# Optimization experiments

Hardware: AMD Instinct MI355X
Metric: run time of the kernel (lower is better)

The kernel has to match this reference:

```python
import jax, jax.numpy as jnp
import numpy as np

B, T = 4, 512
V, D, L, H, F = 32000, 1024, 12, 16, 4096
HD = D // H
CUTS = [0, 2000, 8000, V]
SHRINK = 4


def layer_norm(x, s, b, eps=1e-5):
    m = jnp.mean(x, axis=-1, keepdims=True)
    v = jnp.var(x, axis=-1, keepdims=True)
    return (x - m) * jax.lax.rsqrt(v + eps) * s + b


def rel_shift(x):
    # Transformer-XL relative shift. x: [B, H, T, S] with S == T.
    b, h, t, s = x.shape
    x = jnp.pad(x, ((0, 0), (0, 0), (0, 0), (1, 0)))
    x = x.reshape(b, h, s + 1, t)[:, :, 1:, :]
    return x.reshape(b, h, t, s)


def sinusoid_pos_emb(seq_len, dim):
    # positions seq_len-1 ... 0 (TXL convention), [seq_len, dim]
    pos = jnp.arange(seq_len - 1, -1, -1.0, dtype=jnp.float32)
    inv_freq = 1.0 / (10000.0 ** (jnp.arange(0, dim, 2, dtype=jnp.float32) / dim))
    ang = pos[:, None] * inv_freq[None, :]
    return jnp.concatenate([jnp.sin(ang), jnp.cos(ang)], axis=-1)


def setup_inputs() -> dict:
    key = jax.random.key(0)
    ks = iter(jax.random.split(key, 64))

    def n(shape, std=0.02):
        return jax.random.normal(next(ks), shape, dtype=jnp.float32) * std

    hids = [D // (SHRINK ** i) for i in range(3)]  # 1024, 256, 64
    inp = {}
    inp['x'] = jax.random.randint(next(ks), (B, T), 0, V)
    inp['emb_0'] = n([CUTS[1] - CUTS[0], hids[0]])
    inp['emb_1'] = n([CUTS[2] - CUTS[1], hids[1]])
    inp['emb_2'] = n([CUTS[3] - CUTS[2], hids[2]])
    inp['proj_1'] = n([hids[1], D], 0.01)
    inp['proj_2'] = n([hids[2], D], 0.01)
    inp['out_bias'] = jnp.zeros([V], jnp.float32)
    inp['r_w_bias'] = n([1, 1, H, HD])
    inp['r_r_bias'] = n([1, 1, H, HD])
    inp['ln1_s'] = jnp.ones([L, D], jnp.float32)
    inp['ln1_b'] = jnp.zeros([L, D], jnp.float32)
    inp['Wq'] = n([L, D, D]); inp['bq'] = jnp.zeros([L, D], jnp.float32)
    inp['Wk'] = n([L, D, D]); inp['bk'] = jnp.zeros([L, D], jnp.float32)
    inp['Wv'] = n([L, D, D]); inp['bv'] = jnp.zeros([L, D], jnp.float32)
    inp['Wr'] = n([L, D, D])  # relative position projection (no bias)
    inp['Wo'] = n([L, D, D]); inp['bo'] = jnp.zeros([L, D], jnp.float32)
    inp['ln2_s'] = jnp.ones([L, D], jnp.float32)
    inp['ln2_b'] = jnp.zeros([L, D], jnp.float32)
    inp['W1'] = n([L, D, F]); inp['b1'] = jnp.zeros([L, F], jnp.float32)
    inp['W2'] = n([L, F, D]); inp['b2'] = jnp.zeros([L, D], jnp.float32)
    return inp


def forward(x, emb_0, emb_1, emb_2, proj_1, proj_2, out_bias, r_w_bias, r_r_bias,
            ln1_s, ln1_b, Wq, bq, Wk, bk, Wv, bv, Wr, Wo, bo, ln2_s, ln2_b,
            W1, b1, W2, b2):
    Bx, Tx = x.shape
    # --- adaptive input embedding (clustered table + up-projection, scaled) ---
    embs = [emb_0, emb_1, emb_2]
    projs = [None, proj_1, proj_2]
    h = jnp.zeros((Bx, Tx, D), jnp.float32)
    for i in range(3):
        lo, hi = CUTS[i], CUTS[i + 1]
        in_bucket = (x >= lo) & (x < hi)
        idx = jnp.clip(x - lo, 0, hi - lo - 1)
        e = embs[i][idx]  # [B, T, hid_i]
        if projs[i] is not None:
            e = e @ projs[i]  # -> [B, T, D]
        h = h + jnp.where(in_bucket[..., None], e, 0.0)
    h = h * jnp.sqrt(jnp.float32(D))

    pemb = sinusoid_pos_emb(Tx, D)                  # [T, D]
    causal = jnp.tril(jnp.ones((Tx, Tx), bool))     # [T, T]
    scale = 1.0 / np.sqrt(HD)

    for i in range(L):
        # --- TXL relative-position multi-head attention (pre-norm) ---
        a_in = layer_norm(h, ln1_s[i], ln1_b[i])
        q = (a_in @ Wq[i] + bq[i]).reshape(Bx, Tx, H, HD)
        k = (a_in @ Wk[i] + bk[i]).reshape(Bx, Tx, H, HD)
        v = (a_in @ Wv[i] + bv[i]).reshape(Bx, Tx, H, HD)
        r_k = (pemb @ Wr[i]).reshape(Tx, H, HD)     # [T, H, HD]
        content = jnp.einsum('bthd,bshd->bhts', q + r_w_bias[0, 0], k)
        rel = jnp.einsum('bthd,shd->bhts', q + r_r_bias[0, 0], r_k)
        logits = (content + rel_shift(rel)) * scale
        logits = jnp.where(causal[None, None], logits, jnp.float32(-1e30))
        attn = jax.nn.softmax(logits, axis=-1)
        o = jnp.einsum('bhts,bshd->bthd', attn, v).reshape(Bx, Tx, D)
        h = h + (o @ Wo[i] + bo[i])
        # --- FFN (pre-norm, GELU) ---
        f_in = layer_norm(h, ln2_s[i], ln2_b[i])
        h = h + (jax.nn.gelu(f_in @ W1[i] + b1[i]) @ W2[i] + b2[i])

    # --- tied adaptive-softmax output projection ---
    W_full = jnp.concatenate([emb_0, emb_1 @ proj_1, emb_2 @ proj_2], axis=0)  # [V, D]
    return h @ W_full.T + out_bias  # [B, T, V]


def reference(x, emb_0, emb_1, emb_2, proj_1, proj_2, out_bias, r_w_bias, r_r_bias,
              ln1_s, ln1_b, Wq, bq, Wk, bk, Wv, bv, Wr, Wo, bo, ln2_s, ln2_b,
              W1, b1, W2, b2):
    return forward(x, emb_0, emb_1, emb_2, proj_1, proj_2, out_bias, r_w_bias,
                   r_r_bias, ln1_s, ln1_b, Wq, bq, Wk, bk, Wv, bv, Wr, Wo, bo,
                   ln2_s, ln2_b, W1, b1, W2, b2)
```

## Files before the change

### kernel.cpp

```cpp
#include <hip/hip_runtime.h>

using us = unsigned short;
typedef short short8v __attribute__((ext_vector_type(8)));
typedef float float4v __attribute__((ext_vector_type(4)));

constexpr int NB  = 4;
constexpr int NT  = 512;
constexpr int ND  = 1024;
constexpr int NL  = 12;
constexpr int NH  = 16;
constexpr int NF  = 4096;
constexpr int NHD = 64;
constexpr int NBT = NB * NT;
constexpr int NV  = 32000;
constexpr long QOFF = (long)NBT * ND;
constexpr long RKL  = 640L * 1024;

__device__ __forceinline__ us f2bf(float f) {
    unsigned u = __float_as_uint(f);
    u += 0x7fffu + ((u >> 16) & 1u);
    return (us)(u >> 16);
}

__device__ __forceinline__ void gload16(const us* g, us* l) {
    __builtin_amdgcn_global_load_lds(
        (const __attribute__((address_space(1))) void*)g,
        (__attribute__((address_space(3))) void*)l, 16, 0, 0);
}

template<int BM, int BN, int EPI, bool OUTBF>
__global__ __launch_bounds__(256)
void bgemm_k(const us* __restrict__ A, const us* __restrict__ B, void* Cv,
             const float* __restrict__ bias, const float* addsrc,
             const float* __restrict__ p0, const float* __restrict__ p1,
             us* __restrict__ vtp,
             int N, int K, int lda, int ldb, int ldc,
             int bdiv, long sAb, long sAh, long sBb, long sBh, long sCb, long sCh)
{
    constexpr int BK  = 64;
    constexpr int WTM = BM / 2, WTN = BN / 2;
    constexpr int FM  = WTM / 16, FN = WTN / 16;
    constexpr int AI  = BM / 32;
    constexpr int BI  = BN / 32;
    static_assert(BM % 32 == 0 && BN % 32 == 0, "");

    long coff = 0;
    if (bdiv > 0) {
        int z = blockIdx.z, zb = z / bdiv, zh = z % bdiv;
        A += zb * sAb + zh * sAh;
        B += zb * sBb + zh * sBh;
        coff = zb * sCb + zh * sCh;
    }
    float* Cf = (float*)Cv + coff;
    us*    Ch = (us*)Cv + coff;
    if (addsrc) addsrc += coff;

    __shared__ __align__(16) us As[2 * BM * BK];
    __shared__ __align__(16) us Bs[2 * BN * BK];

    const int tid  = threadIdx.x;
    const int lane = tid & 63;
    const int w    = tid >> 6;
    const int wm   = w >> 1;
    const int wn   = w & 1;
    const int row0 = blockIdx.y * BM;
    const int col0 = blockIdx.x * BN;

    float4v acc[FM][FN];
#pragma unroll
    for (int i = 0; i < FM; ++i)
#pragma unroll
        for (int j = 0; j < FN; ++j) acc[i][j] = (float4v)0.f;

    auto stage = [&](int buf, int k0) {
        us* Ad = As + buf * (BM * BK);
        us* Bd = Bs + buf * (BN * BK);
#pragma unroll
        for (int i = 0; i < AI; ++i) {
            int rb = w * (BM / 4) + i * 8;
            int r  = rb + (lane >> 3);
            int sc8 = ((lane & 7) ^ (r & 7)) << 3;
            gload16(A + (long)(row0 + r) * lda + k0 + sc8, Ad + rb * 64);
        }
#pragma unroll
        for (int i = 0; i < BI; ++i) {
            int rb = w * (BN / 4) + i * 8;
            int r  = rb + (lane >> 3);
            int sc8 = ((lane & 7) ^ (r & 7)) << 3;
            gload16(B + (long)(col0 + r) * ldb + k0 + sc8, Bd + rb * 64);
        }
    };

    stage(0, 0);
    __syncthreads();
    int cur = 0;
    for (int k0 = 0; k0 < K; k0 += BK) {
        if (k0 + BK < K) stage(cur ^ 1, k0 + BK);
        const char* Ac = (const char*)(As + cur * (BM * BK));
        const char* Bc = (const char*)(Bs + cur * (BN * BK));
#pragma unroll
        for (int ks = 0; ks < 2; ++ks) {
            short8v af[FM], bfr[FN];
            int sw = ks * 4 + (lane >> 4);
#pragma unroll
            for (int i = 0; i < FM; ++i) {
                int r = wm * WTM + i * 16 + (lane & 15);
                af[i] = *reinterpret_cast<const short8v*>(Ac + r * 128 + ((sw ^ (r & 7)) << 4));
            }
#pragma unroll
            for (int j = 0; j < FN; ++j) {
                int r = wn * WTN + j * 16 + (lane & 15);
                bfr[j] = *reinterpret_cast<const short8v*>(Bc + r * 128 + ((sw ^ (r & 7)) << 4));
            }
#pragma unroll
            for (int i = 0; i < FM; ++i)
#pragma unroll
                for (int j = 0; j < FN; ++j)
                    acc[i][j] = __builtin_amdgcn_mfma_f32_16x16x32_bf16(af[i], bfr[j], acc[i][j], 0, 0, 0);
        }
        __syncthreads();
        cur ^= 1;
    }

#pragma unroll
    for (int i = 0; i < FM; ++i) {
        int growb = row0 + wm * WTM + i * 16 + ((lane >> 4) << 2);
#pragma unroll
        for (int j = 0; j < FN; ++j) {
            int gcol = col0 + wn * WTN + j * 16 + (lane & 15);
            if (EPI == 3) {
                int seg = gcol >> 10, c = gcol & 1023;
                float bb = bias[gcol];
                if (seg == 2) {
                    unsigned lo = (unsigned)f2bf(acc[i][j][0] + bb)
                                | ((unsigned)f2bf(acc[i][j][1] + bb) << 16);
                    unsigned hi = (unsigned)f2bf(acc[i][j][2] + bb)
                                | ((unsigned)f2bf(acc[i][j][3] + bb) << 16);
                    int bidx = growb >> 9, tb = growb & 511;
                    uint2 pk; pk.x = lo; pk.y = hi;
                    *reinterpret_cast<uint2*>(
                        vtp + ((long)((bidx * 16 + (c >> 6)) * 64 + (c & 63)) << 9) + tb) = pk;
                } else {
                    us* base = (us*)Cv;
#pragma unroll
                    for (int r = 0; r < 4; ++r) {
                        int gr = growb + r;
                        float v = acc[i][j][r] + bb;
                        long o = (long)gr * 1024 + c;
                        if (seg == 0) {
                            base[o]        = f2bf(v + p0[c]);
                            base[o + QOFF] = f2bf(v + p1[c]);
                        } else base[o + 2 * QOFF] = f2bf(v);
                    }
                }
            } else {
                if (gcol >= N) continue;
#pragma unroll
                for (int r = 0; r < 4; ++r) {
                    int gr = growb + r;
                    float v = acc[i][j][r];
                    if (bias) v += bias[gcol];
                    if (EPI == 1) {
                        float xx = v;
                        v = 0.5f * xx * (1.f + tanhf(0.7978845608028654f
                                                     * (xx + 0.044715f * xx * xx * xx)));
                    }
                    if (addsrc) v += addsrc[(long)gr * ldc + gcol];
                    if (OUTBF) Ch[(long)gr * ldc + gcol] = f2bf(v);
                    else       Cf[(long)gr * ldc + gcol] = v;
                }
            }
        }
    }
}

template<int NPART, int MODE>
__global__ __launch_bounds__(256)
void redln_k(const float* __restrict__ part, const float* __restrict__ bias,
             float* __restrict__ h, us* __restrict__ outb,
             const float* __restrict__ sc, const float* __restrict__ bi)
{
    int row = blockIdx.x;
    int d4 = threadIdx.x * 4;
    long i = (long)row * ND + d4;
    float4 hv = *reinterpret_cast<const float4*>(h + i);
    float4 bb = *reinterpret_cast<const float4*>(bias + d4);
    hv.x += bb.x; hv.y += bb.y; hv.z += bb.z; hv.w += bb.w;
#pragma unroll
    for (int z = 0; z < NPART; ++z) {
        float4 a = *reinterpret_cast<const float4*>(part + (long)z * 2097152 + i);
        hv.x += a.x; hv.y += a.y; hv.z += a.z; hv.w += a.w;
    }
    *reinterpret_cast<float4*>(h + i) = hv;
    if (MODE == 1) {
        uint2 p;
        p.x = (unsigned)f2bf(hv.x) | ((unsigned)f2bf(hv.y) << 16);
        p.y = (unsigned)f2bf(hv.z) | ((unsigned)f2bf(hv.w) << 16);
        *reinterpret_cast<uint2*>(outb + i) = p;
    } else {
        float sum = hv.x + hv.y + hv.z + hv.w;
        float sq  = hv.x * hv.x + hv.y * hv.y + hv.z * hv.z + hv.w * hv.w;
#pragma unroll
        for (int o = 32; o; o >>= 1) { sum += __shfl_xor(sum, o); sq += __shfl_xor(sq, o); }
        __shared__ float red[8];
        int w = threadIdx.x >> 6;
        if ((threadIdx.x & 63) == 0) { red[w] = sum; red[4 + w] = sq; }
        __syncthreads();
        sum = red[0] + red[1] + red[2] + red[3];
        sq  = red[4] + red[5] + red[6] + red[7];
        float mean = sum * (1.f / ND);
        float var  = fmaxf(sq * (1.f / ND) - mean * mean, 0.f);
        float inv  = rsqrtf(var + 1e-5f);
        float4 s4 = *reinterpret_cast<const float4*>(&sc[d4]);
        float4 b4 = *reinterpret_cast<const float4*>(&bi[d4]);
        uint2 p;
        p.x = (unsigned)f2bf((hv.x - mean) * inv * s4.x + b4.x)
            | ((unsigned)f2bf((hv.y - mean) * inv * s4.y + b4.y) << 16);
        p.y = (unsigned)f2bf((hv.z - mean) * inv * s4.z + b4.z)
            | ((unsigned)f2bf((hv.w - mean) * inv * s4.w + b4.w) << 16);
        *reinterpret_cast<uint2*>(outb + i) = p;
    }
}

__global__ __launch_bounds__(256)
void fattn_k(const us* __restrict__ qkv, const us* __restrict__ vt,
             const us* __restrict__ rk, us* __restrict__ obuf)
{
    __shared__ __align__(16) us lds_k[64 * 64];
    __shared__ __align__(16) us lds_v[64 * 64];
    __shared__ __align__(16) us lds_rk[64 * 64];
    __shared__ __align__(16) us lds_p[4 * 16 * 64];
    __shared__ float lds_r[4 * 16 * 132];

    const int tid = threadIdx.x, lane = tid & 63, w = tid >> 6;
    const int qtp = blockIdx.x, bh = blockIdx.y;
    const int b = bh >> 4, h = bh & 15;
    const int rg = lane >> 4, lc = lane & 15;

    const us* qwb = qkv + ((long)b * 512) * 1024 + h * 64;
    const us* qrb = qwb + QOFF;
    const us* kb  = qwb + 2 * QOFF;
    const us* vtb = vt + (long)bh * 64 * 512;
    const us* rkb = rk + h * 64;

    float* rbase = lds_r + w * (16 * 132);
    us*    pbase = lds_p + w * (16 * 64);

    for (int hh = 0; hh < 2; ++hh) {
        const int qt = hh ? 7 - qtp : qtp;
        const int t0 = qt * 64;

        short8v aqw[2], aqr[2];
        {
            long qrow = (long)(t0 + w * 16 + lc) * 1024;
            int ko = rg * 8;
            aqw[0] = *(const short8v*)(qwb + qrow + ko);
            aqw[1] = *(const short8v*)(qwb + qrow + 32 + ko);
            aqr[0] = *(const short8v*)(qrb + qrow + ko);
            aqr[1] = *(const short8v*)(qrb + qrow + 32 + ko);
        }

        float4v oacc[4];
#pragma unroll
        for (int i = 0; i < 4; ++i) oacc[i] = (float4v)0.f;
        float mrow[4] = {-3e38f, -3e38f, -3e38f, -3e38f};
        float lrow[4] = {0.f, 0.f, 0.f, 0.f};

        auto stage_rk = [&](int j0) {
#pragma unroll
            for (int i = 0; i < 2; ++i) {
                int rb = w * 16 + i * 8;
                int r  = rb + (lane >> 3);
                int sl = ((lane & 7) ^ (r & 7)) << 3;
                gload16(rkb + (long)(j0 + r) * 1024 + sl, lds_rk + rb * 64);
            }
        };
        auto rel_half = [&](int wbase) {
#pragma unroll
            for (int jn = 0; jn < 4; ++jn) {
                float4v rf = (float4v)0.f;
#pragma unroll
                for (int kk = 0; kk < 2; ++kk) {
                    int r = jn * 16 + lc;
                    int sw = kk * 4 + rg;
                    short8v bf = *(const short8v*)((const char*)lds_rk + r * 128 + ((sw ^ (r & 7)) << 4));
                    rf = __builtin_amdgcn_mfma_f32_16x16x32_bf16(aqr[kk], bf, rf, 0, 0, 0);
                }
#pragma unroll
                for (int pr = 0; pr < 4; ++pr)
                    rbase[(rg * 4 + pr) * 132 + wbase + jn * 16 + lc] = rf[pr];
            }
        };

        const int nst = qt + 1;
        for (int st = 0; st < nst; ++st) {
            const int s0 = st * 64;
            const int jb = (st - qt) * 64 + 448;
            const int sb = ((st - qt + 7) & 1) << 6;

#pragma unroll
            for (int i = 0; i < 2; ++i) {
                int rb = w * 16 + i * 8;
                int r  = rb + (lane >> 3);
                int sl = ((lane & 7) ^ (r & 7)) << 3;
                gload16(kb + (long)(s0 + r) * 1024 + sl, lds_k + rb * 64);
                gload16(vtb + (long)r * 512 + s0 + sl, lds_v + rb * 64);
            }
            if (st == 0) {
                stage_rk(jb);
                __syncthreads();
                rel_half(sb);
                __syncthreads();
                stage_rk(jb + 64);
                __syncthreads();
            } else {
                stage_rk(jb + 64);
                __syncthreads();
            }

            float4v sfr[4];
#pragma unroll
            for (int sn = 0; sn < 4; ++sn) {
                sfr[sn] = (float4v)0.f;
#pragma unroll
                for (int kk = 0; kk < 2; ++kk) {
                    int r = sn * 16 + lc;
                    int sw = kk * 4 + rg;
                    short8v bf = *(const short8v*)((const char*)lds_k + r * 128 + ((sw ^ (r & 7)) << 4));
                    sfr[sn] = __builtin_amdgcn_mfma_f32_16x16x32_bf16(aqw[kk], bf, sfr[sn], 0, 0, 0);
                }
            }
            rel_half(sb ^ 64);

            float pv[4][4];
            float rmax[4] = {-3e38f, -3e38f, -3e38f, -3e38f};
#pragma unroll
            for (int pr = 0; pr < 4; ++pr) {
                int tt = rg * 4 + pr;
                int tw = w * 16 + tt;
#pragma unroll
                for (int sn = 0; sn < 4; ++sn) {
                    int ss = sn * 16 + lc;
                    int slot = (sb + ss + 63 - tw) & 127;
                    float lg = (sfr[sn][pr] + rbase[tt * 132 + slot]) * 0.125f;
                    if (ss > t0 - s0 + tw) lg = -1e30f;
                    pv[sn][pr] = lg;
                    rmax[pr] = fmaxf(rmax[pr], lg);
                }
            }
#pragma unroll
            for (int o = 1; o < 16; o <<= 1)
#pragma unroll
                for (int pr = 0; pr < 4; ++pr)
                    rmax[pr] = fmaxf(rmax[pr], __shfl_xor(rmax[pr], o));
            float rsum[4];
#pragma unroll
            for (int pr = 0; pr < 4; ++pr) {
                float mn = fmaxf(mrow[pr], rmax[pr]);
                float al = __expf(mrow[pr] - mn);
                mrow[pr] = mn;
                lrow[pr] *= al;
                float s = 0.f;
#pragma unroll
                for (int sn = 0; sn < 4; ++sn) {
                    float p = __expf(pv[sn][pr] - mn);
                    pv[sn][pr] = p;
                    s += p;
                }
                rsum[pr] = s;
#pragma unroll
                for (int dn = 0; dn < 4; ++dn) oacc[dn][pr] *= al;
            }
#pragma unroll
            for (int o = 1; o < 16; o <<= 1)
#pragma unroll
                for (int pr = 0; pr < 4; ++pr)
                    rsum[pr] += __shfl_xor(rsum[pr], o);
#pragma unroll
            for (int pr = 0; pr < 4; ++pr) lrow[pr] += rsum[pr];

#pragma unroll
            for (int pr = 0; pr < 4; ++pr) {
                int row = rg * 4 + pr;
#pragma unroll
                for (int sn = 0; sn < 4; ++sn) {
                    int col = sn * 16 + lc;
                    *(us*)((char*)pbase + row * 128 + (((col >> 3) ^ (row & 7)) << 4) + (col & 7) * 2)
                        = f2bf(pv[sn][pr]);
                }
            }
            short8v pa[2];
#pragma unroll
            for (int kk = 0; kk < 2; ++kk)
                pa[kk] = *(const short8v*)((const char*)pbase + lc * 128 + (((kk * 4 + rg) ^ (lc & 7)) << 4));
#pragma unroll
            for (int dn = 0; dn < 4; ++dn) {
#pragma unroll
                for (int kk = 0; kk < 2; ++kk) {
                    int r = dn * 16 + lc;
                    int sw = kk * 4 + rg;
                    short8v vb = *(const short8v*)((const char*)lds_v + r * 128 + ((sw ^ (r & 7)) << 4));
                    oacc[dn] = __builtin_amdgcn_mfma_f32_16x16x32_bf16(pa[kk], vb, oacc[dn], 0, 0, 0);
                }
            }
            __syncthreads();
        }
#pragma unroll
        for (int pr = 0; pr < 4; ++pr) {
            int t = t0 + w * 16 + rg * 4 + pr;
            float inv = 1.f / lrow[pr];
            long rowo = ((long)b * 512 + t) * 1024 + h * 64;
#pragma unroll
            for (int dn = 0; dn < 4; ++dn)
                obuf[rowo + dn * 16 + lc] = f2bf(oacc[dn][pr] * inv);
        }
    }
}

__global__ __launch_bounds__(256)
void tconv_k(const float* __restrict__ in, us* __restrict__ out, int R, int C,
             long inL, long outL)
{
    in  += (long)blockIdx.z * inL;
    out += (long)blockIdx.z * outL;
    __shared__ float t[32][33];
    int c0 = blockIdx.x * 32, r0 = blockIdx.y * 32;
    int tx = threadIdx.x & 31, ty = threadIdx.x >> 5;
#pragma unroll
    for (int j = 0; j < 4; ++j)
        t[ty + j * 8][tx] = in[(long)(r0 + ty + j * 8) * C + c0 + tx];
    __syncthreads();
#pragma unroll
    for (int j = 0; j < 4; ++j)
        out[(long)(c0 + ty + j * 8) * R + r0 + tx] = f2bf(t[tx][ty + j * 8]);
}

__global__ __launch_bounds__(256)
void conv_k(const float* __restrict__ in, us* __restrict__ out, long n)
{
    long i = ((long)blockIdx.x * 256 + threadIdx.x) * 4;
    if (i >= n) return;
    float4 v = *reinterpret_cast<const float4*>(in + i);
    uint2 p;
    p.x = (unsigned)f2bf(v.x) | ((unsigned)f2bf(v.y) << 16);
    p.y = (unsigned)f2bf(v.z) | ((unsigned)f2bf(v.w) << 16);
    *reinterpret_cast<uint2*>(out + i) = p;
}

__global__ __launch_bounds__(256)
void rkpad12_k(us* __restrict__ rk)
{
    int i = blockIdx.x * 256 + threadIdx.x;
    int l = i >> 13, r = i & 8191;
    reinterpret_cast<uint4*>(rk + (long)l * RKL + 512 * 1024)[r] = make_uint4(0, 0, 0, 0);
}

__global__ __launch_bounds__(256)
void bcat_k(const float* __restrict__ bq, const float* __restrict__ bk,
            const float* __restrict__ bv, float* __restrict__ o)
{
    int i = blockIdx.x * 256 + threadIdx.x;
    int l = i / 3072, rr = i % 3072, seg = rr >> 10, c = rr & 1023;
    const float* s = seg == 0 ? bq : seg == 1 ? bk : bv;
    o[i] = s[l * 1024 + c];
}

__global__ __launch_bounds__(256)
void ln_k(const float* __restrict__ x, us* __restrict__ y,
          const float* __restrict__ sc, const float* __restrict__ bi)
{
    int row = blockIdx.x;
    const float* xr = x + (long)row * ND;
    int d4 = threadIdx.x * 4;
    float4 v = *reinterpret_cast<const float4*>(&xr[d4]);
    float sum = v.x + v.y + v.z + v.w;
    float sq  = v.x * v.x + v.y * v.y + v.z * v.z + v.w * v.w;
#pragma unroll
    for (int o = 32; o; o >>= 1) { sum += __shfl_xor(sum, o); sq += __shfl_xor(sq, o); }
    __shared__ float red[8];
    int w = threadIdx.x >> 6;
    if ((threadIdx.x & 63) == 0) { red[w] = sum; red[4 + w] = sq; }
    __syncthreads();
    sum = red[0] + red[1] + red[2] + red[3];
    sq  = red[4] + red[5] + red[6] + red[7];
    float mean = sum * (1.f / ND);
    float var  = fmaxf(sq * (1.f / ND) - mean * mean, 0.f);
    float inv  = rsqrtf(var + 1e-5f);
    float4 s4 = *reinterpret_cast<const float4*>(&sc[d4]);
    float4 b4 = *reinterpret_cast<const float4*>(&bi[d4]);
    uint2 p;
    p.x = (unsigned)f2bf((v.x - mean) * inv * s4.x + b4.x)
        | ((unsigned)f2bf((v.y - mean) * inv * s4.y + b4.y) << 16);
    p.y = (unsigned)f2bf((v.z - mean) * inv * s4.z + b4.z)
        | ((unsigned)f2bf((v.w - mean) * inv * s4.w + b4.w) << 16);
    *reinterpret_cast<uint2*>(y + (long)row * ND + d4) = p;
}

__global__ __launch_bounds__(256)
void pemb_k(us* __restrict__ p)
{
    int t = blockIdx.x;
    float pos = (float)(NT - 1 - t);
    for (int j = threadIdx.x; j < ND / 2; j += 256) {
        float invf = expf(-(float)j * (9.210340371976184f / 512.0f));
        float ang  = pos * invf;
        p[(long)t * ND + j]           = f2bf(sinf(ang));
        p[(long)t * ND + ND / 2 + j]  = f2bf(cosf(ang));
    }
}

__global__ __launch_bounds__(256)
void embed_k(const int* __restrict__ x,
             const float* __restrict__ e0, const float* __restrict__ e1,
             const float* __restrict__ e2, const float* __restrict__ p1,
             const float* __restrict__ p2, float* __restrict__ h)
{
    __shared__ float e[256];
    int tok = blockIdx.x;
    int v = x[tok];
    float* outp = h + (long)tok * ND;
    if (v < 2000) {
        const float* r = e0 + (long)v * ND;
        for (int d = threadIdx.x; d < ND; d += 256) outp[d] = r[d] * 32.0f;
    } else if (v < 8000) {
        const float* r = e1 + (long)(v - 2000) * 256;
        e[threadIdx.x] = r[threadIdx.x];
        __syncthreads();
        for (int d = threadIdx.x; d < ND; d += 256) {
            float acc = 0.f;
#pragma unroll 4
            for (int i = 0; i < 256; ++i) acc += e[i] * p1[(long)i * ND + d];
            outp[d] = acc * 32.0f;
        }
    } else {
        const float* r = e2 + (long)(v - 8000) * 64;
        if (threadIdx.x < 64) e[threadIdx.x] = r[threadIdx.x];
        __syncthreads();
        for (int d = threadIdx.x; d < ND; d += 256) {
            float acc = 0.f;
#pragma unroll 4
            for (int i = 0; i < 64; ++i) acc += e[i] * p2[(long)i * ND + d];
            outp[d] = acc * 32.0f;
        }
    }
}

extern "C" void kernel_launch(void* const* d_in, const int* in_sizes, int n_in,
                              void* d_out, int out_size, void* d_ws, size_t ws_size,
                              hipStream_t stream)
{
    (void)in_sizes; (void)n_in; (void)out_size;
    const int*   x     = (const int*)  d_in[0];
    const float* emb0  = (const float*)d_in[1];
    const float* emb1  = (const float*)d_in[2];
    const float* emb2  = (const float*)d_in[3];
    const float* proj1 = (const float*)d_in[4];
    const float* proj2 = (const float*)d_in[5];
    const float* obias = (const float*)d_in[6];
    const float* rwb   = (const float*)d_in[7];
    const float* rrb   = (const float*)d_in[8];
    const float* ln1s  = (const float*)d_in[9];
    const float* ln1b  = (const float*)d_in[10];
    const float* Wq    = (const float*)d_in[11];
    const float* bq    = (const float*)d_in[12];
    const float* Wk    = (const float*)d_in[13];
    const float* bk    = (const float*)d_in[14];
    const float* Wv    = (const float*)d_in[15];
    const float* bv    = (const float*)d_in[16];
    const float* Wr    = (const float*)d_in[17];
    const float* Wo    = (const float*)d_in[18];
    const float* bo    = (const float*)d_in[19];
    const float* ln2s  = (const float*)d_in[20];
    const float* ln2b  = (const float*)d_in[21];
    const float* W1    = (const float*)d_in[22];
    const float* b1    = (const float*)d_in[23];
    const float* W2    = (const float*)d_in[24];
    const float* b2    = (const float*)d_in[25];
    float* out = (float*)d_out;

    us* ob      = (us*)out;
    us* qkvbuf  = ob;
    us* mid_bf  = ob +  6291456;
    us* vt_bf   = ob + 14680064;
    us* o_bf    = ob + 16777216;
    us* ain_bf  = ob + 18874368;
    us* rk_all  = ob + 20971520;
    us* pemb_bf = ob + 28835840;
    us* wqkv_sc = ob + 29360128;
    us* wr_sc   = ob + 32505856;
    us* wo_sc   = ob + 33554432;
    us* w1_sc   = ob + 34603008;
    us* w2_sc   = ob + 38797312;
    float* pffn = out + 21495808;
    float* pwo  = out + 29884416;

    float* wsf      = (float*)d_ws;
    float* h        = wsf;
    us*    h_bf     = (us*)(wsf + 2097152);
    us*    hp1_bf   = h_bf   + 2097152;
    us*    hp2_bf   = hp1_bf + 524288;
    us*    emb0_bf  = hp2_bf + 131072;
    us*    emb1_bf  = emb0_bf + 2097152;
    us*    emb2_bf  = emb1_bf + 1572864;
    us*    proj1_bf = emb2_bf + 1540096;
    us*    proj2_bf = proj1_bf + 262144;
    float* bqkv     = (float*)(proj2_bf + 65536);
    us*    wqkv_all = (us*)(bqkv + 36864);
    us*    wr_all   = wqkv_all + (long)NL * 3072 * 1024;
    us*    wo_all   = wr_all   + (long)NL * 1024 * 1024;
    us*    w1_all   = wo_all   + (long)NL * 1024 * 1024;
    us*    w2_all   = w1_all   + (long)NL * 4096 * 1024;
    const bool big  = ws_size >= (size_t)352273408;

    bcat_k<<<144, 256, 0, stream>>>(bq, bk, bv, bqkv);
    conv_k<<<2000, 256, 0, stream>>>(emb0,  emb0_bf,  2048000);
    conv_k<<<1500, 256, 0, stream>>>(emb1,  emb1_bf,  1536000);
    conv_k<<<1500, 256, 0, stream>>>(emb2,  emb2_bf,  1536000);
    conv_k<<<256,  256, 0, stream>>>(proj1, proj1_bf, 262144);
    conv_k<<<64,   256, 0, stream>>>(proj2, proj2_bf, 65536);
    pemb_k<<<NT, 256, 0, stream>>>(pemb_bf);
    rkpad12_k<<<384, 256, 0, stream>>>(rk_all);
    embed_k<<<NBT, 256, 0, stream>>>(x, emb0, emb1, emb2, proj1, proj2, h);
    if (big) {
        tconv_k<<<dim3(32, 32, NL), 256, 0, stream>>>(Wq, wqkv_all,           1024, 1024, 1048576, 3145728);
        tconv_k<<<dim3(32, 32, NL), 256, 0, stream>>>(Wk, wqkv_all + 1048576, 1024, 1024, 1048576, 3145728);
        tconv_k<<<dim3(32, 32, NL), 256, 0, stream>>>(Wv, wqkv_all + 2097152, 1024, 1024, 1048576, 3145728);
        tconv_k<<<dim3(32, 32, NL), 256, 0, stream>>>(Wr, wr_all, 1024, 1024, 1048576, 1048576);
        tconv_k<<<dim3(32, 32, NL), 256, 0, stream>>>(Wo, wo_all, 1024, 1024, 1048576, 1048576);
        tconv_k<<<dim3(128, 32, NL), 256, 0, stream>>>(W1, w1_all, 1024, 4096, 4194304, 4194304);
        tconv_k<<<dim3(32, 128, NL), 256, 0, stream>>>(W2, w2_all, 4096, 1024, 4194304, 4194304);
        bgemm_k<64, 64, 0, true><<<dim3(16, 8, NL), 256, 0, stream>>>(
            pemb_bf, wr_all, rk_all, nullptr, nullptr, nullptr, nullptr, nullptr,
            1024, 1024, 1024, 1024, 1024,
            1, 0, 0, 1048576, 0, RKL, 0);
    }
    ln_k<<<NBT, 256, 0, stream>>>(h, ain_bf, ln1s, ln1b);

    for (int l = 0; l < NL; ++l) {
        const us* wqkv_t = big ? wqkv_all + (long)l * 3145728 : wqkv_sc;
        const us* wo_t   = big ? wo_all   + (long)l * 1048576 : wo_sc;
        const us* w1_t   = big ? w1_all   + (long)l * 4194304 : w1_sc;
        const us* w2_t   = big ? w2_all   + (long)l * 4194304 : w2_sc;
        if (!big) {
            const long wOff = (long)l * ND * ND;
            tconv_k<<<dim3(32, 32), 256, 0, stream>>>(Wq + wOff, wqkv_sc,           1024, 1024, 0, 0);
            tconv_k<<<dim3(32, 32), 256, 0, stream>>>(Wk + wOff, wqkv_sc + 1048576, 1024, 1024, 0, 0);
            tconv_k<<<dim3(32, 32), 256, 0, stream>>>(Wv + wOff, wqkv_sc + 2097152, 1024, 1024, 0, 0);
            tconv_k<<<dim3(32, 32), 256, 0, stream>>>(Wr + wOff, wr_sc, 1024, 1024, 0, 0);
            tconv_k<<<dim3(32, 32), 256, 0, stream>>>(Wo + wOff, wo_sc, 1024, 1024, 0, 0);
            tconv_k<<<dim3(128, 32), 256, 0, stream>>>(W1 + (long)l * ND * NF, w1_sc, 1024, 4096, 0, 0);
            tconv_k<<<dim3(32, 128), 256, 0, stream>>>(W2 + (long)l * ND * NF, w2_sc, 4096, 1024, 0, 0);
            bgemm_k<64, 64, 0, true><<<dim3(16, 8, 1), 256, 0, stream>>>(
                pemb_bf, wr_sc, rk_all + (long)l * RKL, nullptr, nullptr, nullptr, nullptr, nullptr,
                1024, 1024, 1024, 1024, 1024, 0, 0, 0, 0, 0, 0, 0);
        }

        bgemm_k<128, 64, 3, true><<<dim3(48, 16, 1), 256, 0, stream>>>(
            ain_bf, wqkv_t, qkvbuf, bqkv + l * 3072, nullptr, rwb, rrb, vt_bf,
            3072, 1024, 1024, 1024, 1024, 0, 0, 0, 0, 0, 0, 0);
        fattn_k<<<dim3(4, NB * NH), 256, 0, stream>>>(
            qkvbuf, vt_bf, rk_all + (long)l * RKL, o_bf);
        bgemm_k<128, 64, 0, false><<<dim3(16, 16, 2), 256, 0, stream>>>(
            o_bf, wo_t, pwo, nullptr, nullptr, nullptr, nullptr, nullptr,
            1024, 512, 1024, 1024, 1024,
            1, 512, 0, 512, 0, 2097152, 0);
        redln_k<2, 0><<<NBT, 256, 0, stream>>>(
            pwo, bo + l * ND, h, ain_bf, ln2s + l * ND, ln2b + l * ND);

        bgemm_k<128, 128, 1, true><<<dim3(32, 16, 1), 256, 0, stream>>>(
            ain_bf, w1_t, mid_bf, b1 + (long)l * NF, nullptr, nullptr, nullptr, nullptr,
            4096, 1024, 1024, 1024, 4096, 0, 0, 0, 0, 0, 0, 0);
        bgemm_k<128, 128, 0, false><<<dim3(8, 16, 4), 256, 0, stream>>>(
            mid_bf, w2_t, pffn, nullptr, nullptr, nullptr, nullptr, nullptr,
            1024, 1024, 4096, 4096, 1024,
            1, 1024, 0, 1024, 0, 2097152, 0);
        if (l < NL - 1)
            redln_k<4, 0><<<NBT, 256, 0, stream>>>(
                pffn, b2 + (long)l * ND, h, ain_bf,
                ln1s + (l + 1) * ND, ln1b + (l + 1) * ND);
        else
            redln_k<4, 1><<<NBT, 256, 0, stream>>>(
                pffn, b2 + (long)l * ND, h, h_bf, nullptr, nullptr);
    }

    bgemm_k<128, 64, 0, false><<<dim3(32, 16, 1), 256, 0, stream>>>(
        h_bf, emb0_bf, out, obias, nullptr, nullptr, nullptr, nullptr,
        2000, 1024, 1024, 1024, NV, 0, 0, 0, 0, 0, 0, 0);
    bgemm_k<64, 64, 0, true><<<dim3(4, 32, 1), 256, 0, stream>>>(
        h_bf, proj1_bf, hp1_bf, nullptr, nullptr, nullptr, nullptr, nullptr,
        256, 1024, 1024, 1024, 256, 0, 0, 0, 0, 0, 0, 0);
    bgemm_k<128, 128, 0, false><<<dim3(47, 16, 1), 256, 0, stream>>>(
        hp1_bf, emb1_bf, out + 2000, obias + 2000, nullptr, nullptr, nullptr, nullptr,
        6000, 256, 256, 256, NV, 0, 0, 0, 0, 0, 0, 0);
    bgemm_k<64, 64, 0, true><<<dim3(1, 32, 1), 256, 0, stream>>>(
        h_bf, proj2_bf, hp2_bf, nullptr, nullptr, nullptr, nullptr, nullptr,
        64, 1024, 1024, 1024, 64, 0, 0, 0, 0, 0, 0, 0);
    bgemm_k<128, 128, 0, false><<<dim3(188, 16, 1), 256, 0, stream>>>(
        hp2_bf, emb2_bf, out + 8000, obias + 8000, nullptr, nullptr, nullptr, nullptr,
        24000, 64, 64, 64, NV, 0, 0, 0, 0, 0, 0, 0);
}
```

Baseline: 2.459 ms.

## Double-buffer K/V and triple-buffer RK tiles in flash attention, merge conversion kernels

The attention kernel now prefetches the next K/V tile and the next relative-key tile into alternate LDS buffers while the current tile is computed, so global loads overlap with MFMA work. This removes the per-iteration barriers that previously serialized load and compute. The five fp32-to-bf16 conversion launches are also merged into one kernel to cut launch overhead. LDS usage roughly doubles for K/V/RK, which may lower occupancy, and the loop relies on the trailing barrier for buffer reuse safety.

```diff
diff --git a/kernel.cpp b/kernel.cpp
--- a/kernel.cpp
+++ b/kernel.cpp
@@ -226,9 +226,9 @@
 void fattn_k(const us* __restrict__ qkv, const us* __restrict__ vt,
              const us* __restrict__ rk, us* __restrict__ obuf)
 {
-    __shared__ __align__(16) us lds_k[64 * 64];
-    __shared__ __align__(16) us lds_v[64 * 64];
-    __shared__ __align__(16) us lds_rk[64 * 64];
+    __shared__ __align__(16) us lds_k[2][64 * 64];
+    __shared__ __align__(16) us lds_v[2][64 * 64];
+    __shared__ __align__(16) us lds_rk[3][64 * 64];
     __shared__ __align__(16) us lds_p[4 * 16 * 64];
     __shared__ float lds_r[4 * 16 * 132];
 
@@ -245,6 +245,26 @@
 
     float* rbase = lds_r + w * (16 * 132);
     us*    pbase = lds_p + w * (16 * 64);
+
+    auto stage_kv = [&](int buf, int s0) {
+#pragma unroll
+        for (int i = 0; i < 2; ++i) {
+            int rb = w * 16 + i * 8;
+            int r  = rb + (lane >> 3);
+            int sl = ((lane & 7) ^ (r & 7)) << 3;
+            gload16(kb + (long)(s0 + r) * 1024 + sl, lds_k[buf] + rb * 64);
+            gload16(vtb + (long)r * 512 + s0 + sl, lds_v[buf] + rb * 64);
+        }
+    };
+    auto stage_rk = [&](int buf, int j0) {
+#pragma unroll
+        for (int i = 0; i < 2; ++i) {
+            int rb = w * 16 + i * 8;
+            int r  = rb + (lane >> 3);
+            int sl = ((lane & 7) ^ (r & 7)) << 3;
+            gload16(rkb + (long)(j0 + r) * 1024 + sl, lds_rk[buf] + rb * 64);
+        }
+    };
 
     for (int hh = 0; hh < 2; ++hh) {
         const int qt = hh ? 7 - qtp : qtp;
@@ -266,16 +286,7 @@
         float mrow[4] = {-3e38f, -3e38f, -3e38f, -3e38f};
         float lrow[4] = {0.f, 0.f, 0.f, 0.f};
 
-        auto stage_rk = [&](int j0) {
-#pragma unroll
-            for (int i = 0; i < 2; ++i) {
-                int rb = w * 16 + i * 8;
-                int r  = rb + (lane >> 3);
-                int sl = ((lane & 7) ^ (r & 7)) << 3;
-                gload16(rkb + (long)(j0 + r) * 1024 + sl, lds_rk + rb * 64);
-            }
-        };
-        auto rel_half = [&](int wbase) {
+        auto rel_half = [&](int buf, int wbase) {
 #pragma unroll
             for (int jn = 0; jn < 4; ++jn) {
                 float4v rf = (float4v)0.f;
@@ -283,7 +294,7 @@
                 for (int kk = 0; kk < 2; ++kk) {
                     int r = jn * 16 + lc;
                     int sw = kk * 4 + rg;
-                    short8v bf = *(const short8v*)((const char*)lds_rk + r * 128 + ((sw ^ (r & 7)) << 4));
+                    short8v bf = *(const short8v*)((const char*)lds_rk[buf] + r * 128 + ((sw ^ (r & 7)) << 4));
                     rf = __builtin_amdgcn_mfma_f32_16x16x32_bf16(aqr[kk], bf, rf, 0, 0, 0);
                 }
 #pragma unroll
@@ -292,32 +303,23 @@
             }
         };
 
-        const int nst = qt + 1;
-        for (int st = 0; st < nst; ++st) {
+        const int jb0 = 448 - qt * 64;
+        stage_kv(0, 0);
+        stage_rk(0, jb0);
+        stage_rk(1, jb0 + 64);
+        __syncthreads();
+
+        for (int st = 0; st <= qt; ++st) {
             const int s0 = st * 64;
-            const int jb = (st - qt) * 64 + 448;
             const int sb = ((st - qt + 7) & 1) << 6;
-
-#pragma unroll
-            for (int i = 0; i < 2; ++i) {
-                int rb = w * 16 + i * 8;
-                int r  = rb + (lane >> 3);
-                int sl = ((lane & 7) ^ (r & 7)) << 3;
-                gload16(kb + (long)(s0 + r) * 1024 + sl, lds_k + rb * 64);
-                gload16(vtb + (long)r * 512 + s0 + sl, lds_v + rb * 64);
-            }
-            if (st == 0) {
-                stage_rk(jb);
-                __syncthreads();
-                rel_half(sb);
-                __syncthreads();
-                stage_rk(jb + 64);
-                __syncthreads();
-            } else {
-                stage_rk(jb + 64);
-                __syncthreads();
-            }
-
+            if (st < qt) {
+                stage_kv((st + 1) & 1, s0 + 64);
+                stage_rk((st + 2) % 3, (st + 1 - qt) * 64 + 448 + 64);
+            }
+            if (st == 0) { rel_half(0, sb); rel_half(1, sb ^ 64); }
+            else         rel_half((st + 1) % 3, sb ^ 64);
+            const char* Kc = (const char*)lds_k[st & 1];
+            const char* Vc = (const char*)lds_v[st & 1];
             float4v sfr[4];
 #pragma unroll
             for (int sn = 0; sn < 4; ++sn) {
@@ -326,11 +328,10 @@
                 for (int kk = 0; kk < 2; ++kk) {
                     int r = sn * 16 + lc;
                     int sw = kk * 4 + rg;
-                    short8v bf = *(const short8v*)((const char*)lds_k + r * 128 + ((sw ^ (r & 7)) << 4));
+                    short8v bf = *(const short8v*)(Kc + r * 128 + ((sw ^ (r & 7)) << 4));
                     sfr[sn] = __builtin_amdgcn_mfma_f32_16x16x32_bf16(aqw[kk], bf, sfr[sn], 0, 0, 0);
                 }
             }
-            rel_half(sb ^ 64);
 
             float pv[4][4];
             float rmax[4] = {-3e38f, -3e38f, -3e38f, -3e38f};
@@ -399,7 +400,7 @@
                 for (int kk = 0; kk < 2; ++kk) {
                     int r = dn * 16 + lc;
                     int sw = kk * 4 + rg;
-                    short8v vb = *(const short8v*)((const char*)lds_v + r * 128 + ((sw ^ (r & 7)) << 4));
+                    short8v vb = *(const short8v*)(Vc + r * 128 + ((sw ^ (r & 7)) << 4));
                     oacc[dn] = __builtin_amdgcn_mfma_f32_16x16x32_bf16(pa[kk], vb, oacc[dn], 0, 0, 0);
                 }
             }
@@ -436,15 +437,25 @@
 }
 
 __global__ __launch_bounds__(256)
-void conv_k(const float* __restrict__ in, us* __restrict__ out, long n)
-{
-    long i = ((long)blockIdx.x * 256 + threadIdx.x) * 4;
-    if (i >= n) return;
-    float4 v = *reinterpret_cast<const float4*>(in + i);
+void convall_k(const float* __restrict__ e0, const float* __restrict__ e1,
+               const float* __restrict__ e2, const float* __restrict__ p1,
+               const float* __restrict__ p2,
+               us* __restrict__ d0, us* __restrict__ d1, us* __restrict__ d2,
+               us* __restrict__ d3, us* __restrict__ d4)
+{
+    int blk = blockIdx.x;
+    const float* s; us* d; long off;
+    if (blk < 2000)      { s = e0; d = d0; off = (long)blk * 1024; }
+    else if (blk < 3500) { s = e1; d = d1; off = (long)(blk - 2000) * 1024; }
+    else if (blk < 5000) { s = e2; d = d2; off = (long)(blk - 3500) * 1024; }
+    else if (blk < 5256) { s = p1; d = d3; off = (long)(blk - 5000) * 1024; }
+    else                 { s = p2; d = d4; off = (long)(blk - 5256) * 1024; }
+    long i = off + (long)threadIdx.x * 4;
+    float4 v = *reinterpret_cast<const float4*>(s + i);
     uint2 p;
     p.x = (unsigned)f2bf(v.x) | ((unsigned)f2bf(v.y) << 16);
     p.y = (unsigned)f2bf(v.z) | ((unsigned)f2bf(v.w) << 16);
-    *reinterpret_cast<uint2*>(out + i) = p;
+    *reinterpret_cast<uint2*>(d + i) = p;
 }
 
 __global__ __launch_bounds__(256)
@@ -613,11 +624,8 @@
     const bool big  = ws_size >= (size_t)352273408;
 
     bcat_k<<<144, 256, 0, stream>>>(bq, bk, bv, bqkv);
-    conv_k<<<2000, 256, 0, stream>>>(emb0,  emb0_bf,  2048000);
-    conv_k<<<1500, 256, 0, stream>>>(emb1,  emb1_bf,  1536000);
-    conv_k<<<1500, 256, 0, stream>>>(emb2,  emb2_bf,  1536000);
-    conv_k<<<256,  256, 0, stream>>>(proj1, proj1_bf, 262144);
-    conv_k<<<64,   256, 0, stream>>>(proj2, proj2_bf, 65536);
+    convall_k<<<5320, 256, 0, stream>>>(emb0, emb1, emb2, proj1, proj2,
+                                        emb0_bf, emb1_bf, emb2_bf, proj1_bf, proj2_bf);
     pemb_k<<<NT, 256, 0, stream>>>(pemb_bf);
     rkpad12_k<<<384, 256, 0, stream>>>(rk_all);
     embed_k<<<NBT, 256, 0, stream>>>(x, emb0, emb1, emb2, proj1, proj2, h);
```

Result: no change. 2.449 ms (-0.4%).

## Split attention KV range across two blocks and merge partial softmax results

Applied to the files above, without the earlier changes.

The flash attention kernel now splits each query tile's key range into two halves across a new grid dimension. Each block writes unnormalised fp32 partial outputs plus row max and sum, and a new merge kernel combines them into bf16 output. This doubles the attention grid from 256 blocks to fuller occupancy on the many-CU GPU, at the cost of extra fp32 global traffic and another launch per layer. Separately, the five embedding conversion launches are fused into a single kernel.

```diff
diff --git a/kernel.cpp b/kernel.cpp
--- a/kernel.cpp
+++ b/kernel.cpp
@@ -224,7 +224,8 @@
 
 __global__ __launch_bounds__(256)
 void fattn_k(const us* __restrict__ qkv, const us* __restrict__ vt,
-             const us* __restrict__ rk, us* __restrict__ obuf)
+             const us* __restrict__ rk, float* __restrict__ pO,
+             float* __restrict__ pm, float* __restrict__ pl)
 {
     __shared__ __align__(16) us lds_k[64 * 64];
     __shared__ __align__(16) us lds_v[64 * 64];
@@ -233,7 +234,7 @@
     __shared__ float lds_r[4 * 16 * 132];
 
     const int tid = threadIdx.x, lane = tid & 63, w = tid >> 6;
-    const int qtp = blockIdx.x, bh = blockIdx.y;
+    const int qtp = blockIdx.x, bh = blockIdx.y, hf = blockIdx.z;
     const int b = bh >> 4, h = bh & 15;
     const int rg = lane >> 4, lc = lane & 15;
 
@@ -246,9 +247,23 @@
     float* rbase = lds_r + w * (16 * 132);
     us*    pbase = lds_p + w * (16 * 64);
 
+    auto stage_rk = [&](int j0) {
+#pragma unroll
+        for (int i = 0; i < 2; ++i) {
+            int rb = w * 16 + i * 8;
+            int r  = rb + (lane >> 3);
+            int sl = ((lane & 7) ^ (r & 7)) << 3;
+            gload16(rkb + (long)(j0 + r) * 1024 + sl, lds_rk + rb * 64);
+        }
+    };
+
     for (int hh = 0; hh < 2; ++hh) {
         const int qt = hh ? 7 - qtp : qtp;
         const int t0 = qt * 64;
+        const int n  = qt + 1;
+        const int h0 = (n + 1) >> 1;
+        const int st_s = hf ? h0 : 0;
+        const int st_e = hf ? n  : h0;
 
         short8v aqw[2], aqr[2];
         {
@@ -266,15 +281,6 @@
         float mrow[4] = {-3e38f, -3e38f, -3e38f, -3e38f};
         float lrow[4] = {0.f, 0.f, 0.f, 0.f};
 
-        auto stage_rk = [&](int j0) {
-#pragma unroll
-            for (int i = 0; i < 2; ++i) {
-                int rb = w * 16 + i * 8;
-                int r  = rb + (lane >> 3);
-                int sl = ((lane & 7) ^ (r & 7)) << 3;
-                gload16(rkb + (long)(j0 + r) * 1024 + sl, lds_rk + rb * 64);
-            }
-        };
         auto rel_half = [&](int wbase) {
 #pragma unroll
             for (int jn = 0; jn < 4; ++jn) {
@@ -292,8 +298,7 @@
             }
         };
 
-        const int nst = qt + 1;
-        for (int st = 0; st < nst; ++st) {
+        for (int st = st_s; st < st_e; ++st) {
             const int s0 = st * 64;
             const int jb = (st - qt) * 64 + 448;
             const int sb = ((st - qt + 7) & 1) << 6;
@@ -306,7 +311,7 @@
                 gload16(kb + (long)(s0 + r) * 1024 + sl, lds_k + rb * 64);
                 gload16(vtb + (long)r * 512 + s0 + sl, lds_v + rb * 64);
             }
-            if (st == 0) {
+            if (st == st_s) {
                 stage_rk(jb);
                 __syncthreads();
                 rel_half(sb);
@@ -405,16 +410,36 @@
             }
             __syncthreads();
         }
+
 #pragma unroll
         for (int pr = 0; pr < 4; ++pr) {
             int t = t0 + w * 16 + rg * 4 + pr;
-            float inv = 1.f / lrow[pr];
-            long rowo = ((long)b * 512 + t) * 1024 + h * 64;
+            long rowi = (long)(hf * 64 + bh) * 512 + t;
+            float* od = pO + rowi * 64;
 #pragma unroll
             for (int dn = 0; dn < 4; ++dn)
-                obuf[rowo + dn * 16 + lc] = f2bf(oacc[dn][pr] * inv);
-        }
-    }
+                od[dn * 16 + lc] = oacc[dn][pr];
+            if (lc == 0) { pm[rowi] = mrow[pr]; pl[rowi] = lrow[pr]; }
+        }
+    }
+}
+
+__global__ __launch_bounds__(256)
+void amerge_k(const float* __restrict__ pO, const float* __restrict__ pm,
+              const float* __restrict__ pl, us* __restrict__ obuf)
+{
+    int row = blockIdx.x * 4 + (threadIdx.x >> 6);
+    int d   = threadIdx.x & 63;
+    float m0 = pm[row], m1 = pm[row + 32768];
+    float l0 = pl[row], l1 = pl[row + 32768];
+    float M  = fmaxf(m0, m1);
+    float a0 = __expf(m0 - M), a1 = __expf(m1 - M);
+    float L  = a0 * l0 + a1 * l1;
+    long i0 = (long)row * 64 + d;
+    float o = (a0 * pO[i0] + a1 * pO[i0 + 2097152]) / L;
+    int bh = row >> 9, t = row & 511;
+    int b = bh >> 4, h = bh & 15;
+    obuf[((long)(b * 512 + t)) * 1024 + h * 64 + d] = f2bf(o);
 }
 
 __global__ __launch_bounds__(256)
@@ -436,15 +461,25 @@
 }
 
 __global__ __launch_bounds__(256)
-void conv_k(const float* __restrict__ in, us* __restrict__ out, long n)
-{
-    long i = ((long)blockIdx.x * 256 + threadIdx.x) * 4;
-    if (i >= n) return;
-    float4 v = *reinterpret_cast<const float4*>(in + i);
+void convall_k(const float* __restrict__ e0, const float* __restrict__ e1,
+               const float* __restrict__ e2, const float* __restrict__ p1,
+               const float* __restrict__ p2,
+               us* __restrict__ d0, us* __restrict__ d1, us* __restrict__ d2,
+               us* __restrict__ d3, us* __restrict__ d4)
+{
+    int blk = blockIdx.x;
+    const float* s; us* d; long off;
+    if (blk < 2000)      { s = e0; d = d0; off = (long)blk * 1024; }
+    else if (blk < 3500) { s = e1; d = d1; off = (long)(blk - 2000) * 1024; }
+    else if (blk < 5000) { s = e2; d = d2; off = (long)(blk - 3500) * 1024; }
+    else if (blk < 5256) { s = p1; d = d3; off = (long)(blk - 5000) * 1024; }
+    else                 { s = p2; d = d4; off = (long)(blk - 5256) * 1024; }
+    long i = off + (long)threadIdx.x * 4;
+    float4 v = *reinterpret_cast<const float4*>(s + i);
     uint2 p;
     p.x = (unsigned)f2bf(v.x) | ((unsigned)f2bf(v.y) << 16);
     p.y = (unsigned)f2bf(v.z) | ((unsigned)f2bf(v.w) << 16);
-    *reinterpret_cast<uint2*>(out + i) = p;
+    *reinterpret_cast<uint2*>(d + i) = p;
 }
 
 __global__ __launch_bounds__(256)
@@ -593,6 +628,9 @@
     us* w2_sc   = ob + 38797312;
     float* pffn = out + 21495808;
     float* pwo  = out + 29884416;
+    float* pO   = out + 34078720;
+    float* pm   = out + 42467328;
+    float* pl   = out + 42532864;
 
     float* wsf      = (float*)d_ws;
     float* h        = wsf;
@@ -613,11 +651,8 @@
     const bool big  = ws_size >= (size_t)352273408;
 
     bcat_k<<<144, 256, 0, stream>>>(bq, bk, bv, bqkv);
-    conv_k<<<2000, 256, 0, stream>>>(emb0,  emb0_bf,  2048000);
-    conv_k<<<1500, 256, 0, stream>>>(emb1,  emb1_bf,  1536000);
-    conv_k<<<1500, 256, 0, stream>>>(emb2,  emb2_bf,  1536000);
-    conv_k<<<256,  256, 0, stream>>>(proj1, proj1_bf, 262144);
-    conv_k<<<64,   256, 0, stream>>>(proj2, proj2_bf, 65536);
+    convall_k<<<5320, 256, 0, stream>>>(emb0, emb1, emb2, proj1, proj2,
+                                        emb0_bf, emb1_bf, emb2_bf, proj1_bf, proj2_bf);
     pemb_k<<<NT, 256, 0, stream>>>(pemb_bf);
     rkpad12_k<<<384, 256, 0, stream>>>(rk_all);
     embed_k<<<NBT, 256, 0, stream>>>(x, emb0, emb1, emb2, proj1, proj2, h);
@@ -658,8 +693,9 @@
         bgemm_k<128, 64, 3, true><<<dim3(48, 16, 1), 256, 0, stream>>>(
             ain_bf, wqkv_t, qkvbuf, bqkv + l * 3072, nullptr, rwb, rrb, vt_bf,
             3072, 1024, 1024, 1024, 1024, 0, 0, 0, 0, 0, 0, 0);
-        fattn_k<<<dim3(4, NB * NH), 256, 0, stream>>>(
-            qkvbuf, vt_bf, rk_all + (long)l * RKL, o_bf);
+        fattn_k<<<dim3(4, NB * NH, 2), 256, 0, stream>>>(
+            qkvbuf, vt_bf, rk_all + (long)l * RKL, pO, pm, pl);
+        amerge_k<<<8192, 256, 0, stream>>>(pO, pm, pl, o_bf);
         bgemm_k<128, 64, 0, false><<<dim3(16, 16, 2), 256, 0, stream>>>(
             o_bf, wo_t, pwo, nullptr, nullptr, nullptr, nullptr, nullptr,
             1024, 512, 1024, 1024, 1024,
```

New measurement: 2.465 ms. No clear change (+0.2%).
